# Performance work log

Hardware: AMD Instinct MI355X
Metric: run time of the kernel (lower is better)

Reference implementation:

```python
import jax, jax.numpy as jnp
import numpy as np

N_NODES = 100000
N_EDGES = 1600000
D_IN = 128
D_OUT = 128


def setup_inputs() -> dict:
    key = jax.random.key(0)
    ks = jax.random.split(key, 6)
    x = jax.random.normal(ks[0], (N_NODES, D_IN), dtype=jnp.float32)
    edge_row = jax.random.randint(ks[1], (N_EDGES,), 0, N_NODES, dtype=jnp.int32)
    edge_col = jax.random.randint(ks[2], (N_EDGES,), 0, N_NODES, dtype=jnp.int32)
    # normalized adjacency values (e.g. 1/deg), roughly uniform small positives
    edge_val = jax.random.uniform(ks[3], (N_EDGES,), dtype=jnp.float32) * (1.0 / 16.0)
    # torch Linear weight is [out,in]; we store transposed [in,out] for x @ W
    scale = float(np.sqrt(6.0 / (D_IN + D_OUT)))  # xavier_uniform
    W_local = jax.random.uniform(ks[4], (D_IN, D_OUT), dtype=jnp.float32, minval=-scale, maxval=scale)
    W_neigh = jax.random.uniform(ks[5], (D_IN, D_OUT), dtype=jnp.float32, minval=-scale, maxval=scale)
    b_local = jnp.zeros((D_OUT,), dtype=jnp.float32)
    b_neigh = jnp.zeros((D_OUT,), dtype=jnp.float32)
    return {"x": x, "edge_row": edge_row, "edge_col": edge_col, "edge_val": edge_val,
            "W_local": W_local, "b_local": b_local, "W_neigh": W_neigh, "b_neigh": b_neigh}


def reference(x, edge_row, edge_col, edge_val, W_local, b_local, W_neigh, b_neigh):
    # feat_trans_local = linear_local(x)
    local = x @ W_local + b_local  # [N, D_OUT]
    # sparse.mm(edge_norm, x): out[r] += val * x[c]  (COO SpMM via gather + segment_sum)
    msgs = edge_val[:, None] * x[edge_col]  # [E, D_IN]
    agg = jax.ops.segment_sum(msgs, edge_row, num_segments=N_NODES)  # [N, D_IN]
    neigh = agg @ W_neigh + b_neigh  # [N, D_OUT]
    out = jnp.concatenate([local, neigh], axis=1)  # [N, 2*D_OUT]
    return jax.nn.relu(out)
```

## Files before the change

kernel.cpp:

```cpp
#include <hip/hip_runtime.h>
#include <hip/hip_bf16.h>

#define D 128
#define WPAD 136
#define RPC 64
#define RPC_SHIFT 6
#define RPB 8
#define CAPC 1280
#define NCMAX 2048
#define P1_BLOCKS 256

typedef __attribute__((ext_vector_type(8))) short short8;
typedef __attribute__((ext_vector_type(8))) __bf16 bf16x8;
typedef __attribute__((ext_vector_type(4))) float float4_t;

__device__ __forceinline__ short f2bf(float f) {
    __hip_bfloat16 b = __float2bfloat16(f);
    return __builtin_bit_cast(short, b);
}

__device__ __forceinline__ short8 load_frag8(const float* p) {
    const float4_t* q = reinterpret_cast<const float4_t*>(p);
    float4_t u = q[0], v = q[1];
    short8 r;
    r[0] = f2bf(u[0]); r[1] = f2bf(u[1]); r[2] = f2bf(u[2]); r[3] = f2bf(u[3]);
    r[4] = f2bf(v[0]); r[5] = f2bf(v[1]); r[6] = f2bf(v[2]); r[7] = f2bf(v[3]);
    return r;
}

__device__ __forceinline__ float4_t mfma_bf16(short8 a, short8 b, float4_t c) {
    return __builtin_amdgcn_mfma_f32_16x16x32_bf16(
        __builtin_bit_cast(bf16x8, a), __builtin_bit_cast(bf16x8, b), c, 0, 0, 0);
}

__device__ __forceinline__ float bf_lo(unsigned u) { return __uint_as_float(u << 16); }
__device__ __forceinline__ float bf_hi(unsigned u) { return __uint_as_float(u & 0xFFFF0000u); }

__global__ __launch_bounds__(256) void gemm_kernel(
    const float* __restrict__ x,
    const float* __restrict__ Wl, const float* __restrict__ bl,
    const float* __restrict__ Wn,
    float* __restrict__ out, unsigned short* __restrict__ y,
    int* __restrict__ gcur, int ncoarse, int N)
{
    __shared__ short lW[D * WPAD];

    int gid = blockIdx.x * 256 + threadIdx.x;
    if (gid < ncoarse) gcur[gid] = 0;

    for (int i = threadIdx.x; i < D * D; i += 256) {
        int k = i >> 7, n = i & (D - 1);
        lW[n * WPAD + k] = f2bf(Wl[i]);
    }

    int wave = threadIdx.x >> 6;
    int lane = threadIdx.x & 63;
    int quad = lane >> 4;
    int l16  = lane & 15;
    int rbase = blockIdx.x * 128 + wave * 32;

    short8 ax[2][4];
    for (int m = 0; m < 2; ++m) {
        int row  = rbase + m * 16 + l16;
        int rowc = row < N ? row : N - 1;
        const float* xp = x + (size_t)rowc * D + quad * 8;
        for (int t = 0; t < 4; ++t) ax[m][t] = load_frag8(xp + t * 32);
    }
    __syncthreads();

    for (int nt = 0; nt < 8; ++nt) {
        int colc = nt * 16 + l16;
        float4_t acc[2];
        acc[0] = acc[1] = (float4_t){0.f, 0.f, 0.f, 0.f};
        const short* bp = lW + colc * WPAD + quad * 8;
        for (int t = 0; t < 4; ++t) {
            short8 bf = *reinterpret_cast<const short8*>(bp + t * 32);
            acc[0] = mfma_bf16(ax[0][t], bf, acc[0]);
            acc[1] = mfma_bf16(ax[1][t], bf, acc[1]);
        }
        float bLc = bl[colc];
        for (int m = 0; m < 2; ++m) {
            int row0 = rbase + m * 16 + quad * 4;
            for (int i = 0; i < 4; ++i) {
                int rr = row0 + i;
                if (rr < N) {
                    float lv = acc[m][i] + bLc;
                    out[(size_t)rr * 256 + colc] = lv > 0.f ? lv : 0.f;
                }
            }
        }
    }
    __syncthreads();

    for (int i = threadIdx.x; i < D * D; i += 256) {
        int k = i >> 7, n = i & (D - 1);
        lW[n * WPAD + k] = f2bf(Wn[i]);
    }
    __syncthreads();

    for (int nt = 0; nt < 8; ++nt) {
        int colc = nt * 16 + l16;
        float4_t acc[2];
        acc[0] = acc[1] = (float4_t){0.f, 0.f, 0.f, 0.f};
        const short* bp = lW + colc * WPAD + quad * 8;
        for (int t = 0; t < 4; ++t) {
            short8 bf = *reinterpret_cast<const short8*>(bp + t * 32);
            acc[0] = mfma_bf16(ax[0][t], bf, acc[0]);
            acc[1] = mfma_bf16(ax[1][t], bf, acc[1]);
        }
        for (int m = 0; m < 2; ++m) {
            int row0 = rbase + m * 16 + quad * 4;
            for (int i = 0; i < 4; ++i) {
                int rr = row0 + i;
                if (rr < N)
                    y[(size_t)rr * D + colc] = (unsigned short)f2bf(acc[m][i]);
            }
        }
    }
}

__global__ __launch_bounds__(256) void coarse_scatter(
    const int* __restrict__ erow, const int* __restrict__ ecol,
    const float* __restrict__ eval, int* __restrict__ gcur,
    int2* __restrict__ pairs1, int E, int ncoarse)
{
    __shared__ int hist[NCMAX];
    __shared__ int base[NCMAX];
    int tid = threadIdx.x;
    for (int i = tid; i < ncoarse; i += 256) hist[i] = 0;
    __syncthreads();

    int chunk = (E + P1_BLOCKS - 1) / P1_BLOCKS;
    int e0 = blockIdx.x * chunk;
    int e1 = e0 + chunk; e1 = e1 < E ? e1 : E;

    for (int e = e0 + tid; e < e1; e += 256)
        atomicAdd(&hist[erow[e] >> RPC_SHIFT], 1);
    __syncthreads();

    for (int i = tid; i < ncoarse; i += 256) {
        int h = hist[i];
        base[i] = h ? atomicAdd(&gcur[i], h) : 0;
        hist[i] = 0;
    }
    __syncthreads();

    for (int e = e0 + tid; e < e1; e += 256) {
        int r = erow[e];
        int c = r >> RPC_SHIFT;
        int pos = atomicAdd(&hist[c], 1) + base[c];
        if (pos < CAPC) {
            int key = ((r & (RPC - 1)) << 17) | ecol[e];
            pairs1[(size_t)c * CAPC + pos] = make_int2(key, __float_as_int(eval[e]));
        }
    }
}

__global__ __launch_bounds__(256) void bucket_gather(
    const unsigned short* __restrict__ y, const int* __restrict__ gcur,
    const int2* __restrict__ pairs1, const float* __restrict__ bn,
    float* __restrict__ out, int N)
{
    __shared__ float accall[4 * RPB * D];
    __shared__ unsigned short bidx[CAPC];
    __shared__ int hist[8];
    __shared__ int off[8];
    __shared__ int cur[8];
    __shared__ float bnl[D];

    int tid  = threadIdx.x;
    int wave = tid >> 6;
    int lane = tid & 63;
    int c    = blockIdx.x;

    if (tid < 8) { hist[tid] = 0; cur[tid] = 0; }
    if (tid < D) bnl[tid] = bn[tid];
    __syncthreads();

    int cnt = gcur[c];
    cnt = cnt < CAPC ? cnt : CAPC;
    const int2* pb = pairs1 + (size_t)c * CAPC;

    for (int j = tid; j < cnt; j += 256)
        atomicAdd(&hist[(pb[j].x >> 20) & 7], 1);
    __syncthreads();

    if (tid == 0) {
        int run = 0;
        for (int g = 0; g < 8; ++g) { off[g] = run; run += hist[g]; }
    }
    __syncthreads();

    for (int j = tid; j < cnt; j += 256) {
        int g = (pb[j].x >> 20) & 7;
        int pos = atomicAdd(&cur[g], 1) + off[g];
        bidx[pos] = (unsigned short)j;
    }
    __syncthreads();

    const unsigned* yv = reinterpret_cast<const unsigned*>(y);
    float* plane = accall + wave * (RPB * D);
    float4_t z = {0.f, 0.f, 0.f, 0.f};

    for (int gg = 0; gg < 2; ++gg) {
        int g = wave * 2 + gg;

        for (int i = lane; i < RPB * (D / 4); i += 64)
            reinterpret_cast<float4_t*>(plane)[i] = z;

        int j0 = off[g];
        int j1 = j0 + hist[g];
        int j = j0;
        for (; j + 7 < j1; j += 8) {
            int2 p[8];
            unsigned t[8];
            #pragma unroll
            for (int u = 0; u < 8; ++u) p[u] = pb[bidx[j + u]];
            #pragma unroll
            for (int u = 0; u < 8; ++u)
                t[u] = yv[(size_t)(p[u].x & 0x1FFFF) * 64 + lane];
            #pragma unroll
            for (int u = 0; u < 8; ++u) {
                float v = __int_as_float(p[u].y);
                float* a = plane + (((unsigned)p[u].x >> 17) & 7) * D + lane * 2;
                float2 o = *reinterpret_cast<float2*>(a);
                o.x += v * bf_lo(t[u]); o.y += v * bf_hi(t[u]);
                *reinterpret_cast<float2*>(a) = o;
            }
        }
        for (; j < j1; ++j) {
            int2 p = pb[bidx[j]];
            unsigned t = yv[(size_t)(p.x & 0x1FFFF) * 64 + lane];
            float v = __int_as_float(p.y);
            float* a = plane + (((unsigned)p.x >> 17) & 7) * D + lane * 2;
            float2 o = *reinterpret_cast<float2*>(a);
            o.x += v * bf_lo(t); o.y += v * bf_hi(t);
            *reinterpret_cast<float2*>(a) = o;
        }

        int nodebase = c * RPC + g * RPB;
        for (int r = 0; r < RPB; ++r) {
            int node = nodebase + r;
            if (node < N) {
                float s0 = plane[r * D + lane * 2]     + bnl[lane * 2];
                float s1 = plane[r * D + lane * 2 + 1] + bnl[lane * 2 + 1];
                float2 ov;
                ov.x = s0 > 0.f ? s0 : 0.f;
                ov.y = s1 > 0.f ? s1 : 0.f;
                reinterpret_cast<float2*>(out + (size_t)node * 256 + D)[lane] = ov;
            }
        }
    }
}

extern "C" void kernel_launch(void* const* d_in, const int* in_sizes, int n_in,
                              void* d_out, int out_size, void* d_ws, size_t ws_size,
                              hipStream_t stream) {
    const float* x    = (const float*)d_in[0];
    const int*   erow = (const int*)  d_in[1];
    const int*   ecol = (const int*)  d_in[2];
    const float* eval = (const float*)d_in[3];
    const float* Wl   = (const float*)d_in[4];
    const float* bl   = (const float*)d_in[5];
    const float* Wn   = (const float*)d_in[6];
    const float* bn   = (const float*)d_in[7];
    float*       out  = (float*)d_out;

    int N = in_sizes[0] / D;
    int E = in_sizes[1];
    int ncoarse = (N + RPC - 1) >> RPC_SHIFT;

    char* ws = (char*)d_ws;
    size_t off_y   = 0;
    size_t off_p1  = off_y  + (size_t)N * D * sizeof(short);
    size_t off_gc  = off_p1 + (size_t)ncoarse * CAPC * sizeof(int2);

    unsigned short* y = (unsigned short*)(ws + off_y);
    int2* pairs1 = (int2*)(ws + off_p1);
    int*  gcur   = (int*)(ws + off_gc);

    int gblocks = (N + 127) / 128;
    gemm_kernel<<<gblocks, 256, 0, stream>>>(x, Wl, bl, Wn, out, y, gcur, ncoarse, N);

    coarse_scatter<<<P1_BLOCKS, 256, 0, stream>>>(erow, ecol, eval, gcur, pairs1, E, ncoarse);

    bucket_gather<<<ncoarse, 256, 0, stream>>>(y, gcur, pairs1, bn, out, N);
}
```

Before: 337.2 us.

## Sort bucket edges per row and accumulate in registers instead of LDS planes

The gather kernel now counting-sorts each bucket's edges by individual row (64 groups) instead of by 8-row group. Each wave then processes one row at a time, keeping its accumulators in registers, so the LDS accumulation planes and their read-modify-write traffic go away. The trade-offs are a serial 64-entry prefix scan on a single thread, an unroll that drops from 8 to 4 (fewer gathers in flight), and more frequent short tail loops, since each row has only about 16 edges.

```diff
diff --git a/kernel.cpp b/kernel.cpp
--- a/kernel.cpp
+++ b/kernel.cpp
@@ -5,7 +5,6 @@
 #define WPAD 136
 #define RPC 64
 #define RPC_SHIFT 6
-#define RPB 8
 #define CAPC 1280
 #define NCMAX 2048
 #define P1_BLOCKS 256
@@ -161,20 +160,17 @@
     const int2* __restrict__ pairs1, const float* __restrict__ bn,
     float* __restrict__ out, int N)
 {
-    __shared__ float accall[4 * RPB * D];
     __shared__ unsigned short bidx[CAPC];
-    __shared__ int hist[8];
-    __shared__ int off[8];
-    __shared__ int cur[8];
-    __shared__ float bnl[D];
+    __shared__ int hist[RPC];
+    __shared__ int off[RPC];
+    __shared__ int cur[RPC];
 
     int tid  = threadIdx.x;
     int wave = tid >> 6;
     int lane = tid & 63;
     int c    = blockIdx.x;
 
-    if (tid < 8) { hist[tid] = 0; cur[tid] = 0; }
-    if (tid < D) bnl[tid] = bn[tid];
+    if (tid < RPC) { hist[tid] = 0; cur[tid] = 0; }
     __syncthreads();
 
     int cnt = gcur[c];
@@ -182,73 +178,61 @@
     const int2* pb = pairs1 + (size_t)c * CAPC;
 
     for (int j = tid; j < cnt; j += 256)
-        atomicAdd(&hist[(pb[j].x >> 20) & 7], 1);
+        atomicAdd(&hist[(pb[j].x >> 17) & (RPC - 1)], 1);
     __syncthreads();
 
     if (tid == 0) {
         int run = 0;
-        for (int g = 0; g < 8; ++g) { off[g] = run; run += hist[g]; }
+        for (int g = 0; g < RPC; ++g) { off[g] = run; run += hist[g]; }
     }
     __syncthreads();
 
     for (int j = tid; j < cnt; j += 256) {
-        int g = (pb[j].x >> 20) & 7;
+        int g = (pb[j].x >> 17) & (RPC - 1);
         int pos = atomicAdd(&cur[g], 1) + off[g];
         bidx[pos] = (unsigned short)j;
     }
     __syncthreads();
 
     const unsigned* yv = reinterpret_cast<const unsigned*>(y);
-    float* plane = accall + wave * (RPB * D);
-    float4_t z = {0.f, 0.f, 0.f, 0.f};
-
-    for (int gg = 0; gg < 2; ++gg) {
-        int g = wave * 2 + gg;
-
-        for (int i = lane; i < RPB * (D / 4); i += 64)
-            reinterpret_cast<float4_t*>(plane)[i] = z;
-
+    float2 bnv = reinterpret_cast<const float2*>(bn)[lane];
+
+    for (int rr = 0; rr < RPC / 4; ++rr) {
+        int g  = wave * (RPC / 4) + rr;
         int j0 = off[g];
-        int j1 = j0 + hist[g];
-        int j = j0;
-        for (; j + 7 < j1; j += 8) {
-            int2 p[8];
-            unsigned t[8];
-            #pragma unroll
-            for (int u = 0; u < 8; ++u) p[u] = pb[bidx[j + u]];
-            #pragma unroll
-            for (int u = 0; u < 8; ++u)
-                t[u] = yv[(size_t)(p[u].x & 0x1FFFF) * 64 + lane];
-            #pragma unroll
-            for (int u = 0; u < 8; ++u) {
-                float v = __int_as_float(p[u].y);
-                float* a = plane + (((unsigned)p[u].x >> 17) & 7) * D + lane * 2;
-                float2 o = *reinterpret_cast<float2*>(a);
-                o.x += v * bf_lo(t[u]); o.y += v * bf_hi(t[u]);
-                *reinterpret_cast<float2*>(a) = o;
-            }
-        }
-        for (; j < j1; ++j) {
-            int2 p = pb[bidx[j]];
+        int n  = hist[g];
+        float a0x = 0.f, a0y = 0.f, a1x = 0.f, a1y = 0.f;
+        int j = 0;
+        for (; j + 3 < n; j += 4) {
+            int2 p0 = pb[bidx[j0 + j    ]];
+            int2 p1 = pb[bidx[j0 + j + 1]];
+            int2 p2 = pb[bidx[j0 + j + 2]];
+            int2 p3 = pb[bidx[j0 + j + 3]];
+            unsigned t0 = yv[(size_t)(p0.x & 0x1FFFF) * 64 + lane];
+            unsigned t1 = yv[(size_t)(p1.x & 0x1FFFF) * 64 + lane];
+            unsigned t2 = yv[(size_t)(p2.x & 0x1FFFF) * 64 + lane];
+            unsigned t3 = yv[(size_t)(p3.x & 0x1FFFF) * 64 + lane];
+            float v0 = __int_as_float(p0.y), v1 = __int_as_float(p1.y);
+            float v2 = __int_as_float(p2.y), v3 = __int_as_float(p3.y);
+            a0x += v0 * bf_lo(t0); a0y += v0 * bf_hi(t0);
+            a1x += v1 * bf_lo(t1); a1y += v1 * bf_hi(t1);
+            a0x += v2 * bf_lo(t2); a0y += v2 * bf_hi(t2);
+            a1x += v3 * bf_lo(t3); a1y += v3 * bf_hi(t3);
+        }
+        for (; j < n; ++j) {
+            int2 p = pb[bidx[j0 + j]];
             unsigned t = yv[(size_t)(p.x & 0x1FFFF) * 64 + lane];
             float v = __int_as_float(p.y);
-            float* a = plane + (((unsigned)p.x >> 17) & 7) * D + lane * 2;
-            float2 o = *reinterpret_cast<float2*>(a);
-            o.x += v * bf_lo(t); o.y += v * bf_hi(t);
-            *reinterpret_cast<float2*>(a) = o;
-        }
-
-        int nodebase = c * RPC + g * RPB;
-        for (int r = 0; r < RPB; ++r) {
-            int node = nodebase + r;
-            if (node < N) {
-                float s0 = plane[r * D + lane * 2]     + bnl[lane * 2];
-                float s1 = plane[r * D + lane * 2 + 1] + bnl[lane * 2 + 1];
-                float2 ov;
-                ov.x = s0 > 0.f ? s0 : 0.f;
-                ov.y = s1 > 0.f ? s1 : 0.f;
-                reinterpret_cast<float2*>(out + (size_t)node * 256 + D)[lane] = ov;
-            }
+            a0x += v * bf_lo(t); a0y += v * bf_hi(t);
+        }
+        int node = c * RPC + g;
+        if (node < N) {
+            float s0 = a0x + a1x + bnv.x;
+            float s1 = a0y + a1y + bnv.y;
+            float2 ov;
+            ov.x = s0 > 0.f ? s0 : 0.f;
+            ov.y = s1 > 0.f ? s1 : 0.f;
+            reinterpret_cast<float2*>(out + (size_t)node * 256 + D)[lane] = ov;
         }
     }
 }
```

New measurement: 330.3 us. 2.0% less time.
